# Kernel optimization log

Measured on AMD Instinct MI355X. Metric: run time of the kernel, lower is better.

Reference implementation:

```python
import jax, jax.numpy as jnp
import numpy as np

B, L, D, K = 16, 512, 512, 8
D2 = 2 * D
KS = 9
PAD = (KS - 1) // 2
EPS = 1e-5


def _conv_block(x, w, b, g, beta):
    # x: [B, L, D]; conv over time dim with 'same' padding, then LayerNorm over D, ReLU
    y = jax.lax.conv_general_dilated(
        x.transpose(0, 2, 1), w, window_strides=(1,), padding=[(PAD, PAD)],
        dimension_numbers=('NCH', 'OIH', 'NCH'))
    y = y.transpose(0, 2, 1) + b  # [B, L, D]
    mean = jnp.mean(y, axis=-1, keepdims=True)
    var = jnp.var(y, axis=-1, keepdims=True)
    y = (y - mean) * jax.lax.rsqrt(var + EPS) * g + beta
    return jax.nn.relu(y)


def _gru_scan(x, w_ih, w_hh, b_ih, b_hh):
    # x: [B, L, D]; torch GRUCell math, input = concat(x_t, h_{t-1}) per module
    def step(h, x_t):
        p = jnp.concatenate([x_t, h], axis=-1)          # [B, D + D2]
        gi = p @ w_ih.T + b_ih                          # [B, 3*D2]
        gh = h @ w_hh.T + b_hh
        ir, iz, inn = jnp.split(gi, 3, axis=-1)
        hr, hz, hn = jnp.split(gh, 3, axis=-1)
        r = jax.nn.sigmoid(ir + hr)
        z = jax.nn.sigmoid(iz + hz)
        n = jnp.tanh(inn + r * hn)
        h_new = (1.0 - z) * n + z * h
        return h_new, h_new

    h0 = jnp.zeros((x.shape[0], w_hh.shape[1]), x.dtype)
    _, hs = jax.lax.scan(step, h0, x.transpose(1, 0, 2))  # [L, B, D2]
    return hs.transpose(1, 0, 2)                           # [B, L, D2]


def setup_inputs() -> dict:
    key = jax.random.key(0)
    ks = jax.random.split(key, 12)
    n = lambda k, sh, s=0.02: jax.random.normal(k, sh, dtype=jnp.float32) * s
    return {
        'h_text': jax.random.normal(ks[0], (B, L, D), dtype=jnp.float32),
        'conv1_w': n(ks[1], (D, D, KS)), 'conv1_b': jnp.zeros((D,), jnp.float32),
        'ln1_g': jnp.ones((D,), jnp.float32), 'ln1_b': jnp.zeros((D,), jnp.float32),
        'conv2_w': n(ks[2], (D, D, KS)), 'conv2_b': jnp.zeros((D,), jnp.float32),
        'ln2_g': jnp.ones((D,), jnp.float32), 'ln2_b': jnp.zeros((D,), jnp.float32),
        'w_ih': n(ks[3], (3 * D2, D + D2)), 'w_hh': n(ks[4], (3 * D2, D2)),
        'b_ih': jnp.zeros((3 * D2,), jnp.float32), 'b_hh': jnp.zeros((3 * D2,), jnp.float32),
        'mdn_w_w': n(ks[5], (K, D2)), 'mdn_w_b': jnp.zeros((K,), jnp.float32),
        'mdn_sigma_w': n(ks[6], (K * D2, D2)), 'mdn_sigma_b': jnp.zeros((K * D2,), jnp.float32),
        'mdn_mu_w': n(ks[7], (K * D2, D2)), 'mdn_mu_b': jnp.zeros((K * D2,), jnp.float32),
    }


def reference(h_text, conv1_w, conv1_b, ln1_g, ln1_b, conv2_w, conv2_b, ln2_g, ln2_b,
              w_ih, w_hh, b_ih, b_hh, mdn_w_w, mdn_w_b, mdn_sigma_w, mdn_sigma_b,
              mdn_mu_w, mdn_mu_b):
    x = _conv_block(h_text, conv1_w, conv1_b, ln1_g, ln1_b)
    x = _conv_block(x, conv2_w, conv2_b, ln2_g, ln2_b)
    h = _gru_scan(x, w_ih, w_hh, b_ih, b_hh)                 # [B, L, 2D]
    w = jax.nn.softmax(h @ mdn_w_w.T + mdn_w_b, axis=-1)     # [B, L, K]
    sigma = jnp.exp(h @ mdn_sigma_w.T + mdn_sigma_b).reshape(B, L, K, D2)
    mu = (h @ mdn_mu_w.T + mdn_mu_b).reshape(B, L, K, D2)
    return (w, sigma, mu)
```

## Files before the change

kernel.cpp:

```cpp
#include <hip/hip_runtime.h>
#include <hip/hip_bf16.h>
#include <math.h>

#define BB 16
#define LL 512
#define DD 512
#define DD2 1024
#define KMIX 8
#define LPAD 520
#define GRU_KSTEPS 33

typedef __attribute__((ext_vector_type(8))) short short8;
typedef __attribute__((ext_vector_type(4))) float f32x4;
typedef unsigned short ushort;

__device__ __forceinline__ float bf2f(ushort u) {
  union { float f; unsigned i; } v; v.i = ((unsigned)u) << 16; return v.f;
}
__device__ __forceinline__ ushort f2bf(float f) {
  union { float f; unsigned i; } v; v.f = f;
  unsigned i = v.i;
  unsigned r = i + 0x7FFF + ((i >> 16) & 1);
  return (ushort)(r >> 16);
}

__global__ void k_zero_bf16(ushort* p, long n) {
  for (long i = blockIdx.x * 256 + threadIdx.x; i < n; i += (long)gridDim.x * 256) p[i] = 0;
}
__global__ void k_fill_xpad(const float* __restrict__ x, ushort* __restrict__ xp) {
  const long n = (long)BB * LPAD * DD;
  for (long i = blockIdx.x * 256 + threadIdx.x; i < n; i += (long)gridDim.x * 256) {
    int d = (int)(i & 511);
    long rest = i >> 9;
    int p = (int)(rest % LPAD);
    int b = (int)(rest / LPAD);
    float v = 0.f;
    if (p >= 4 && p < 516) v = x[((long)b * LL + (p - 4)) * DD + d];
    xp[i] = f2bf(v);
  }
}
__global__ void k_pack_convw(const float* __restrict__ w, ushort* __restrict__ wp) {
  const long n = (long)DD * DD * 9;
  for (long idx = blockIdx.x * 256 + threadIdx.x; idx < n; idx += (long)gridDim.x * 256) {
    int i = (int)(idx & 511);
    int o = (int)((idx >> 9) & 511);
    int k = (int)(idx >> 18);
    wp[idx] = f2bf(w[((long)o * DD + i) * 9 + k]);
  }
}
__global__ void k_pack_wihx(const float* __restrict__ w_ih, ushort* __restrict__ wp) {
  const long n = (long)3 * DD2 * DD;
  for (long idx = blockIdx.x * 256 + threadIdx.x; idx < n; idx += (long)gridDim.x * 256) {
    int i = (int)(idx & 511);
    int nr = (int)(idx >> 9);
    wp[idx] = f2bf(w_ih[(long)nr * 1536 + i]);
  }
}
__global__ void k_pack_bf16(const float* __restrict__ s, ushort* __restrict__ d, long n) {
  for (long i = blockIdx.x * 256 + threadIdx.x; i < n; i += (long)gridDim.x * 256) d[i] = f2bf(s[i]);
}
__global__ void k_pack_gru(const float* __restrict__ w_ih, const float* __restrict__ w_hh,
                           const float* __restrict__ b_hh, ushort* __restrict__ wp) {
  const long n = (long)64 * 6 * GRU_KSTEPS * 64 * 8;
  for (long idx = blockIdx.x * 256 + threadIdx.x; idx < n; idx += (long)gridDim.x * 256) {
    int j = (int)(idx & 7);
    int lane = (int)((idx >> 3) & 63);
    long r9 = idx >> 9;
    int ks = (int)(r9 % GRU_KSTEPS);
    long tmp = r9 / GRU_KSTEPS;
    int s = (int)(tmp % 6);
    int blk = (int)(tmp / 6);
    int k = ks * 32 + ((lane >> 4) << 3) + j;
    int u = blk * 16 + (lane & 15);
    float v = 0.f;
    if (s < 3) {
      if (k < 1024) v = w_ih[((long)(s * DD2 + u)) * 1536 + 512 + k];
    } else {
      int nr = (s - 3) * DD2 + u;
      if (k < 1024) v = w_hh[(long)nr * DD2 + k];
      else if (k == 1024) v = b_hh[nr];
    }
    wp[idx] = f2bf(v);
  }
}
__global__ void k_init_hbuf(ushort* hb, unsigned* flags) {
  int i = blockIdx.x * 256 + threadIdx.x;
  if (i < 16384) hb[i] = 0;
  if (i < 1024) flags[i] = 0u;
}

__global__ __launch_bounds__(256) void conv_gemm(
    const ushort* __restrict__ A, const ushort* __restrict__ Bt,
    float* __restrict__ Cout, const float* __restrict__ bias) {
  __shared__ ushort As[64 * 64];
  __shared__ ushort Bs[128 * 64];
  const int tid = threadIdx.x, lane = tid & 63, w = tid >> 6;
  const int wr = w >> 1, wc = w & 1;
  const int m0 = blockIdx.y * 64, n0 = blockIdx.x * 128;
  const int b = m0 >> 9, l = m0 & 511;
  const ushort* Abase = A + ((long)(b * LPAD + l)) * DD;
  const ushort* Bbase = Bt + (long)n0 * DD;

  f32x4 acc[2][4];
#pragma unroll
  for (int m = 0; m < 2; m++)
#pragma unroll
    for (int n = 0; n < 4; n++) acc[m][n] = {0.f, 0.f, 0.f, 0.f};

  for (int seg = 0; seg < 9; ++seg) {
    const ushort* Aseg = Abase + (long)seg * DD;
    const ushort* Bseg = Bbase + (long)seg * DD * DD;
    for (int k0 = 0; k0 < DD; k0 += 64) {
#pragma unroll
      for (int it = 0; it < 2; ++it) {
        int chunk = it * 256 + tid;
        int r = chunk >> 3, cc = chunk & 7, sc = cc ^ (r & 7);
        *(short8*)&As[(size_t)chunk * 8] = *(const short8*)(Aseg + (long)r * DD + k0 + sc * 8);
      }
#pragma unroll
      for (int it = 0; it < 4; ++it) {
        int chunk = it * 256 + tid;
        int r = chunk >> 3, cc = chunk & 7, sc = cc ^ (r & 7);
        *(short8*)&Bs[(size_t)chunk * 8] = *(const short8*)(Bseg + (long)r * DD + k0 + sc * 8);
      }
      __syncthreads();
#pragma unroll
      for (int kk = 0; kk < 2; ++kk) {
        short8 af[2], bfv[4];
#pragma unroll
        for (int m = 0; m < 2; m++) {
          int row = wr * 32 + m * 16 + (lane & 15);
          int ch = (kk * 4 + (lane >> 4)) ^ (row & 7);
          af[m] = *(const short8*)&As[(size_t)(row * 8 + ch) * 8];
        }
#pragma unroll
        for (int nn = 0; nn < 4; nn++) {
          int row = wc * 64 + nn * 16 + (lane & 15);
          int ch = (kk * 4 + (lane >> 4)) ^ (row & 7);
          bfv[nn] = *(const short8*)&Bs[(size_t)(row * 8 + ch) * 8];
        }
#pragma unroll
        for (int m = 0; m < 2; m++)
#pragma unroll
          for (int nn = 0; nn < 4; nn++)
            acc[m][nn] = __builtin_amdgcn_mfma_f32_16x16x32_bf16(af[m], bfv[nn], acc[m][nn], 0, 0, 0);
      }
      __syncthreads();
    }
  }
#pragma unroll
  for (int nn = 0; nn < 4; nn++) {
    const int c = n0 + wc * 64 + nn * 16 + (lane & 15);
    const float bv = bias[c];
#pragma unroll
    for (int m = 0; m < 2; m++) {
      const int rbase = m0 + wr * 32 + m * 16 + ((lane >> 4) << 2);
#pragma unroll
      for (int j = 0; j < 4; j++)
        Cout[(long)(rbase + j) * DD + c] = acc[m][nn][j] + bv;
    }
  }
}

__global__ __launch_bounds__(256) void gix_gemm(
    const ushort* __restrict__ A, const ushort* __restrict__ Bt,
    ushort* __restrict__ Cout, const float* __restrict__ bias) {
  __shared__ ushort As[128 * 64];
  __shared__ ushort Bs[128 * 64];
  const int tid = threadIdx.x, lane = tid & 63, w = tid >> 6;
  const int wr = w >> 1, wc = w & 1;
  const int m0 = blockIdx.y * 128, n0 = blockIdx.x * 128;
  const ushort* Abase = A + (long)m0 * DD;
  const ushort* Bbase = Bt + (long)n0 * DD;

  f32x4 acc[4][4];
#pragma unroll
  for (int i = 0; i < 4; i++)
#pragma unroll
    for (int j = 0; j < 4; j++) acc[i][j] = {0.f, 0.f, 0.f, 0.f};

  for (int k0 = 0; k0 < DD; k0 += 64) {
#pragma unroll
    for (int it = 0; it < 4; ++it) {
      int chunk = it * 256 + tid;
      int r = chunk >> 3, cc = chunk & 7, sc = cc ^ (r & 7);
      *(short8*)&As[(size_t)chunk * 8] = *(const short8*)(Abase + (long)r * DD + k0 + sc * 8);
      *(short8*)&Bs[(size_t)chunk * 8] = *(const short8*)(Bbase + (long)r * DD + k0 + sc * 8);
    }
    __syncthreads();
#pragma unroll
    for (int kk = 0; kk < 2; ++kk) {
      short8 af[4], bfv[4];
#pragma unroll
      for (int m = 0; m < 4; m++) {
        int row = wr * 64 + m * 16 + (lane & 15);
        int ch = (kk * 4 + (lane >> 4)) ^ (row & 7);
        af[m] = *(const short8*)&As[(size_t)(row * 8 + ch) * 8];
      }
#pragma unroll
      for (int nn = 0; nn < 4; nn++) {
        int row = wc * 64 + nn * 16 + (lane & 15);
        int ch = (kk * 4 + (lane >> 4)) ^ (row & 7);
        bfv[nn] = *(const short8*)&Bs[(size_t)(row * 8 + ch) * 8];
      }
#pragma unroll
      for (int m = 0; m < 4; m++)
#pragma unroll
        for (int nn = 0; nn < 4; nn++)
          acc[m][nn] = __builtin_amdgcn_mfma_f32_16x16x32_bf16(af[m], bfv[nn], acc[m][nn], 0, 0, 0);
    }
    __syncthreads();
  }
#pragma unroll
  for (int m = 0; m < 4; m++) {
    int rbase = m0 + wr * 64 + m * 16 + ((lane >> 4) << 2);
#pragma unroll
    for (int nn = 0; nn < 4; nn++) {
      int c = n0 + wc * 64 + nn * 16 + (lane & 15);
      const float bv = bias[c];
#pragma unroll
      for (int j = 0; j < 4; j++) {
        float v = acc[m][nn][j] + bv;
        int r = rbase + j;
        int bb = r >> 9, tt = r & 511, ss = c >> 10, uu = c & 1023;
        long o2 = ((((long)(tt * 64 + (uu >> 4))) * 3 + ss) << 8) + (bb << 4) + (uu & 15);
        Cout[o2] = f2bf(v);
      }
    }
  }
}

template <int DSTPAD>
__global__ __launch_bounds__(256) void ln_relu(
    const float* __restrict__ y, const float* __restrict__ g,
    const float* __restrict__ be, ushort* __restrict__ dst) {
  const int r = blockIdx.x, tid = threadIdx.x;
  float v0 = y[(long)r * DD + tid];
  float v1 = y[(long)r * DD + 256 + tid];
  float s = v0 + v1, sq = v0 * v0 + v1 * v1;
#pragma unroll
  for (int o = 32; o; o >>= 1) { s += __shfl_down(s, o); sq += __shfl_down(sq, o); }
  __shared__ float red[8];
  int w = tid >> 6, lane = tid & 63;
  if (lane == 0) { red[w] = s; red[4 + w] = sq; }
  __syncthreads();
  if (tid == 0) {
    float ts = 0.f, tq = 0.f;
#pragma unroll
    for (int i = 0; i < 4; i++) { ts += red[i]; tq += red[4 + i]; }
    red[0] = ts; red[1] = tq;
  }
  __syncthreads();
  float mean = red[0] * (1.f / 512.f);
  float var = red[1] * (1.f / 512.f) - mean * mean;
  float rs = rsqrtf(var + 1e-5f);
  long dbase;
  if (DSTPAD) { int b = r >> 9, l = r & 511; dbase = ((long)(b * LPAD + l + 4)) * DD; }
  else dbase = (long)r * DD;
  float o0 = fmaxf(0.f, (v0 - mean) * rs * g[tid] + be[tid]);
  float o1 = fmaxf(0.f, (v1 - mean) * rs * g[tid + 256] + be[tid + 256]);
  dst[dbase + tid] = f2bf(o0);
  dst[dbase + 256 + tid] = f2bf(o1);
}

__device__ __forceinline__ void wait_flags(unsigned need, int tid,
                                           const unsigned* __restrict__ flags) {
  if ((tid >> 6) == 0) {
    while (1) {
      unsigned f = __hip_atomic_load(&flags[(tid & 63) << 4], __ATOMIC_RELAXED,
                                     __HIP_MEMORY_SCOPE_AGENT);
      if (__all((int)(f >= need))) break;
      __builtin_amdgcn_s_sleep(127);
    }
  }
  __syncthreads();
}

template <int MR>
__device__ void do_pair(int m0, int n0,
                        const ushort* __restrict__ A,
                        const ushort* __restrict__ Bsg, const ushort* __restrict__ Bmu,
                        const float* __restrict__ sg_b, const float* __restrict__ mu_b,
                        float* __restrict__ Cs, float* __restrict__ Cm,
                        char* smem, int tid) {
  constexpr int NF = (MR == 128) ? 2 : 1;
  ushort* As = (ushort*)smem;
  ushort* B1 = As + MR * 64;
  ushort* B2 = B1 + 128 * 64;
  const int lane = tid & 63, w = tid >> 6;
  const int wr = (MR == 128) ? (w >> 2) : 0;
  const int wc = (MR == 128) ? (w & 3) : w;
  const ushort* Abase = A + (long)m0 * DD2;
  const ushort* Bsb = Bsg + (long)n0 * DD2;
  const ushort* Bmb = Bmu + (long)n0 * DD2;
  f32x4 accS[4][NF], accM[4][NF];
#pragma unroll
  for (int m = 0; m < 4; m++)
#pragma unroll
    for (int n = 0; n < NF; n++) { accS[m][n] = {0.f,0.f,0.f,0.f}; accM[m][n] = {0.f,0.f,0.f,0.f}; }

  for (int k0 = 0; k0 < DD2; k0 += 64) {
#pragma unroll
    for (int it = 0; it < MR / 64; ++it) {
      int chunk = it * 512 + tid;
      int r = chunk >> 3, cc = chunk & 7, sc = cc ^ (r & 7);
      *(short8*)&As[(size_t)chunk * 8] = *(const short8*)(Abase + (long)r * DD2 + k0 + sc * 8);
    }
#pragma unroll
    for (int it = 0; it < 2; ++it) {
      int chunk = it * 512 + tid;
      int r = chunk >> 3, cc = chunk & 7, sc = cc ^ (r & 7);
      *(short8*)&B1[(size_t)chunk * 8] = *(const short8*)(Bsb + (long)r * DD2 + k0 + sc * 8);
      *(short8*)&B2[(size_t)chunk * 8] = *(const short8*)(Bmb + (long)r * DD2 + k0 + sc * 8);
    }
    __syncthreads();
#pragma unroll
    for (int kk = 0; kk < 2; ++kk) {
      short8 af[4], b1[NF], b2[NF];
#pragma unroll
      for (int m = 0; m < 4; m++) {
        int row = wr * 64 + m * 16 + (lane & 15);
        int ch = (kk * 4 + (lane >> 4)) ^ (row & 7);
        af[m] = *(const short8*)&As[(size_t)(row * 8 + ch) * 8];
      }
#pragma unroll
      for (int n = 0; n < NF; n++) {
        int row = wc * (16 * NF) + n * 16 + (lane & 15);
        int ch = (kk * 4 + (lane >> 4)) ^ (row & 7);
        b1[n] = *(const short8*)&B1[(size_t)(row * 8 + ch) * 8];
        b2[n] = *(const short8*)&B2[(size_t)(row * 8 + ch) * 8];
      }
#pragma unroll
      for (int m = 0; m < 4; m++)
#pragma unroll
        for (int n = 0; n < NF; n++) {
          accS[m][n] = __builtin_amdgcn_mfma_f32_16x16x32_bf16(af[m], b1[n], accS[m][n], 0, 0, 0);
          accM[m][n] = __builtin_amdgcn_mfma_f32_16x16x32_bf16(af[m], b2[n], accM[m][n], 0, 0, 0);
        }
    }
    __syncthreads();
  }
  const int ldc = KMIX * DD2;
#pragma unroll
  for (int n = 0; n < NF; n++) {
    const int c = n0 + wc * (16 * NF) + n * 16 + (lane & 15);
    const float bs = sg_b[c], bm = mu_b[c];
#pragma unroll
    for (int m = 0; m < 4; m++) {
      const int rbase = m0 + wr * 64 + m * 16 + ((lane >> 4) << 2);
#pragma unroll
      for (int j = 0; j < 4; j++) {
        const long off = (long)(rbase + j) * ldc + c;
        Cs[off] = expf(accS[m][n][j] + bs);
        Cm[off] = accM[m][n][j] + bm;
      }
    }
  }
}

__global__ __launch_bounds__(512, 2) void fused_scan_mdn(
    const ushort* __restrict__ Wp, const ushort* __restrict__ gix2,
    const float* __restrict__ b_hh,
    ushort* __restrict__ hbuf, ushort* __restrict__ h_seq,
    unsigned* __restrict__ flags,
    const ushort* __restrict__ mdnsg, const ushort* __restrict__ mdnmu,
    const float* __restrict__ sg_b, const float* __restrict__ mu_b,
    float* __restrict__ outS, float* __restrict__ outM,
    const float* __restrict__ ww, const float* __restrict__ wb,
    float* __restrict__ outW) {
  __shared__ char smem[49152];
  const int tid = threadIdx.x;

  if (blockIdx.x < 64) {
    float* red = (float*)smem;
    const int lane = tid & 63, w = tid >> 6, blk = blockIdx.x;
    const int j_c = w;
    const int u_local = lane & 15;
    const int b = ((lane >> 4) << 2) + (j_c & 3);
    const int u = (blk << 4) + u_local;
    const int lanep = ((blk & 1) * 2 + (u_local >> 3)) * 16 + b;
    const long hout_off = ((long)(blk >> 1) * 64 + lanep) * 8 + (u_local & 7);
    const ushort* wpw = Wp + (long)blk * 6 * GRU_KSTEPS * 512 + (long)lane * 8;
    const float bhr = b_hh[u], bhz = b_hh[DD2 + u], bhn = b_hh[2 * DD2 + u];
    float hold = 0.f;

    short8 wr0[4], wr1[4], wr2[4], wr3[4], wr4[4], wr5[4];
#pragma unroll
    for (int i = 0; i < 4; ++i) {
      const int ks = i * 8 + w;
      wr0[i] = *(const short8*)(wpw + (long)(0 * GRU_KSTEPS + ks) * 512);
      wr1[i] = *(const short8*)(wpw + (long)(1 * GRU_KSTEPS + ks) * 512);
      wr2[i] = *(const short8*)(wpw + (long)(2 * GRU_KSTEPS + ks) * 512);
      wr3[i] = *(const short8*)(wpw + (long)(3 * GRU_KSTEPS + ks) * 512);
      wr4[i] = *(const short8*)(wpw + (long)(4 * GRU_KSTEPS + ks) * 512);
      wr5[i] = *(const short8*)(wpw + (long)(5 * GRU_KSTEPS + ks) * 512);
    }

    const int gofs = (b << 4) + u_local;
    for (int t = 0; t < LL; ++t) {
      float gx_r = 0.f, gx_z = 0.f, gx_n = 0.f;
      if (w < 4) {
        const long gbase = ((long)(t * 64 + blk) * 3) << 8;
        gx_r = bf2f(__builtin_nontemporal_load(gix2 + gbase + gofs));
        gx_z = bf2f(__builtin_nontemporal_load(gix2 + gbase + 256 + gofs));
        gx_n = bf2f(__builtin_nontemporal_load(gix2 + gbase + 512 + gofs));
      }
      if (t > 0) {
        if (w == 0) {
          const unsigned tgt = (unsigned)t;
          while (1) {
            unsigned f = __hip_atomic_load(&flags[lane << 4], __ATOMIC_RELAXED,
                                           __HIP_MEMORY_SCOPE_AGENT);
            if (__all((int)(f >= tgt))) break;
            __builtin_amdgcn_s_sleep(1);
          }
        }
        __syncthreads();
      }

      const ushort* hb = hbuf + ((long)t << 14);
      f32x4 acc0 = {0.f,0.f,0.f,0.f}, acc1 = acc0, acc2 = acc0,
            acc3 = acc0, acc4 = acc0, acc5 = acc0;
#pragma unroll
      for (int i = 0; i < 4; ++i) {
        const int ks = i * 8 + w;
        unsigned long long* ap = (unsigned long long*)(hb + (((long)ks * 64 + lane) << 3));
        union { unsigned long long q[2]; short8 v; } cv;
        cv.q[0] = __hip_atomic_load(ap,     __ATOMIC_RELAXED, __HIP_MEMORY_SCOPE_AGENT);
        cv.q[1] = __hip_atomic_load(ap + 1, __ATOMIC_RELAXED, __HIP_MEMORY_SCOPE_AGENT);
        acc0 = __builtin_amdgcn_mfma_f32_16x16x32_bf16(cv.v, wr0[i], acc0, 0, 0, 0);
        acc1 = __builtin_amdgcn_mfma_f32_16x16x32_bf16(cv.v, wr1[i], acc1, 0, 0, 0);
        acc2 = __builtin_amdgcn_mfma_f32_16x16x32_bf16(cv.v, wr2[i], acc2, 0, 0, 0);
        acc3 = __builtin_amdgcn_mfma_f32_16x16x32_bf16(cv.v, wr3[i], acc3, 0, 0, 0);
        acc4 = __builtin_amdgcn_mfma_f32_16x16x32_bf16(cv.v, wr4[i], acc4, 0, 0, 0);
        acc5 = __builtin_amdgcn_mfma_f32_16x16x32_bf16(cv.v, wr5[i], acc5, 0, 0, 0);
      }
#pragma unroll
      for (int j = 0; j < 4; ++j) {
        red[((w * 6 + 0) << 8) + (j << 6) + lane] = acc0[j];
        red[((w * 6 + 1) << 8) + (j << 6) + lane] = acc1[j];
        red[((w * 6 + 2) << 8) + (j << 6) + lane] = acc2[j];
        red[((w * 6 + 3) << 8) + (j << 6) + lane] = acc3[j];
        red[((w * 6 + 4) << 8) + (j << 6) + lane] = acc4[j];
        red[((w * 6 + 5) << 8) + (j << 6) + lane] = acc5[j];
      }
      __syncthreads();
      ushort h16 = 0;
      if (w < 4) {
        float v0 = 0.f, v1 = 0.f, v2 = 0.f, v3 = 0.f, v4 = 0.f, v5 = 0.f;
#pragma unroll
        for (int wv = 0; wv < 8; ++wv) {
          const int base = ((wv * 6) << 8) + (j_c << 6) + lane;
          v0 += red[base];
          v1 += red[base + 256];
          v2 += red[base + 512];
          v3 += red[base + 768];
          v4 += red[base + 1024];
          v5 += red[base + 1280];
        }
        const float rg = 1.f / (1.f + __expf(-(gx_r + v0 + v3 + bhr)));
        const float zg = 1.f / (1.f + __expf(-(gx_z + v1 + v4 + bhz)));
        const float nx = gx_n + v2 + rg * (v5 + bhn);
        const float ng = 1.f - 2.f / (__expf(2.f * nx) + 1.f);
        const float hn = (1.f - zg) * ng + zg * hold;
        hold = hn;
        h16 = f2bf(hn);
      }
      if (t < LL - 1) {
        if (w < 4)
          __hip_atomic_store(hbuf + (((long)(t + 1)) << 14) + hout_off, h16,
                             __ATOMIC_RELAXED, __HIP_MEMORY_SCOPE_AGENT);
        __syncthreads();
        if (tid == 0)
          __hip_atomic_store(&flags[blk << 4], (unsigned)(t + 1), __ATOMIC_RELAXED,
                             __HIP_MEMORY_SCOPE_AGENT);
      }
      if (w < 4)
        __hip_atomic_store(h_seq + ((long)b * LL + t) * DD2 + u, h16,
                           __ATOMIC_RELAXED, __HIP_MEMORY_SCOPE_AGENT);
    }
    __syncthreads();
    if (tid == 0)
      __hip_atomic_store(&flags[blk << 4], 600u, __ATOMIC_RELAXED,
                         __HIP_MEMORY_SCOPE_AGENT);
  } else {
    const int wid = blockIdx.x - 64;
    for (int i = wid; i < 3072; i += 192) {
      const int nb = i & 63;
      const int rest = i >> 6;
      const int b = rest & 15;
      const int t0 = (rest >> 4) * 128;
      wait_flags((unsigned)(t0 + 129), tid, flags);
      do_pair<128>(b * 512 + t0, nb * 128, h_seq, mdnsg, mdnmu, sg_b, mu_b,
                   outS, outM, smem, tid);
    }
    for (int i = wid; i < 1024; i += 192) {
      const int nb = i & 63;
      const int b = (i >> 6) & 15;
      wait_flags(449u, tid, flags);
      do_pair<64>(b * 512 + 384, nb * 128, h_seq, mdnsg, mdnmu, sg_b, mu_b,
                  outS, outM, smem, tid);
    }
  }
  for (int i = blockIdx.x; i < 1024; i += 256) {
    const int nb = i & 63;
    const int b = (i >> 6) & 15;
    wait_flags(513u, tid, flags);
    do_pair<64>(b * 512 + 448, nb * 128, h_seq, mdnsg, mdnmu, sg_b, mu_b,
                outS, outM, smem, tid);
  }
  wait_flags(513u, tid, flags);
  {
    const int lane = tid & 63, w = tid >> 6;
#pragma unroll
    for (int i = 0; i < 4; ++i) {
      const long r = (long)blockIdx.x * 32 + i * 8 + w;
      float s[KMIX];
#pragma unroll
      for (int k = 0; k < KMIX; k++) s[k] = 0.f;
      for (int u = lane; u < DD2; u += 64) {
        float hv = bf2f(h_seq[r * DD2 + u]);
#pragma unroll
        for (int k = 0; k < KMIX; k++) s[k] += hv * ww[(long)k * DD2 + u];
      }
#pragma unroll
      for (int k = 0; k < KMIX; k++)
#pragma unroll
        for (int o = 32; o; o >>= 1) s[k] += __shfl_xor(s[k], o);
#pragma unroll
      for (int k = 0; k < KMIX; k++) s[k] += wb[k];
      float m = s[0];
#pragma unroll
      for (int k = 1; k < KMIX; k++) m = fmaxf(m, s[k]);
      float esum = 0.f;
#pragma unroll
      for (int k = 0; k < KMIX; k++) { s[k] = expf(s[k] - m); esum += s[k]; }
      float mine = 0.f;
#pragma unroll
      for (int k = 0; k < KMIX; k++) if (lane == k) mine = s[k];
      if (lane < KMIX) outW[r * KMIX + lane] = mine / esum;
    }
  }
}

extern "C" void kernel_launch(void* const* d_in, const int* in_sizes, int n_in,
                              void* d_out, int out_size, void* d_ws, size_t ws_size,
                              hipStream_t stream) {
  const float* h_text     = (const float*)d_in[0];
  const float* conv1_w    = (const float*)d_in[1];
  const float* conv1_b    = (const float*)d_in[2];
  const float* ln1_g      = (const float*)d_in[3];
  const float* ln1_b      = (const float*)d_in[4];
  const float* conv2_w    = (const float*)d_in[5];
  const float* conv2_b    = (const float*)d_in[6];
  const float* ln2_g      = (const float*)d_in[7];
  const float* ln2_b      = (const float*)d_in[8];
  const float* w_ih       = (const float*)d_in[9];
  const float* w_hh       = (const float*)d_in[10];
  const float* b_ih       = (const float*)d_in[11];
  const float* b_hh       = (const float*)d_in[12];
  const float* mdn_w_w    = (const float*)d_in[13];
  const float* mdn_w_b    = (const float*)d_in[14];
  const float* mdn_sig_w  = (const float*)d_in[15];
  const float* mdn_sig_b  = (const float*)d_in[16];
  const float* mdn_mu_w   = (const float*)d_in[17];
  const float* mdn_mu_b   = (const float*)d_in[18];
  float* out = (float*)d_out;

  char* ws = (char*)d_ws;
  size_t off = 0;
  auto take = [&](size_t bytes) {
    void* p = ws + off;
    off += (bytes + 255) & ~(size_t)255;
    return p;
  };
  ushort* xpad1  = (ushort*)take((size_t)BB * LPAD * DD * 2);
  ushort* xpad2  = (ushort*)take((size_t)BB * LPAD * DD * 2);
  ushort* wpack1 = (ushort*)take((size_t)DD * DD * 9 * 2);
  ushort* wpack2 = (ushort*)take((size_t)DD * DD * 9 * 2);
  float*  ybuf   = (float*) take((size_t)BB * LL * DD * 4);
  ushort* x2     = (ushort*)take((size_t)BB * LL * DD * 2);
  ushort* wihx   = (ushort*)take((size_t)3 * DD2 * DD * 2);
  ushort* gix    = (ushort*)take((size_t)BB * LL * 3 * DD2 * 2);
  ushort* Wp     = (ushort*)take((size_t)64 * 6 * GRU_KSTEPS * 64 * 8 * 2);
  ushort* hseq   = (ushort*)take((size_t)BB * LL * DD2 * 2);
  ushort* mdnmu  = (ushort*)take((size_t)KMIX * DD2 * DD2 * 2);
  ushort* mdnsg  = (ushort*)take((size_t)KMIX * DD2 * DD2 * 2);
  ushort* hbuf   = (ushort*)take((size_t)512 * 16384 * 2);
  unsigned* flags = (unsigned*)take(64 * 16 * 4);

  const long sigma_off = (long)BB * LL * KMIX;
  const long mu_off    = sigma_off + (long)BB * LL * KMIX * DD2;

  k_fill_xpad<<<2048, 256, 0, stream>>>(h_text, xpad1);
  k_zero_bf16<<<2048, 256, 0, stream>>>(xpad2, (long)BB * LPAD * DD);
  k_pack_convw<<<2048, 256, 0, stream>>>(conv1_w, wpack1);
  k_pack_convw<<<2048, 256, 0, stream>>>(conv2_w, wpack2);
  k_pack_wihx<<<2048, 256, 0, stream>>>(w_ih, wihx);
  k_pack_gru<<<2048, 256, 0, stream>>>(w_ih, w_hh, b_hh, Wp);
  k_pack_bf16<<<2048, 256, 0, stream>>>(mdn_mu_w, mdnmu, (long)KMIX * DD2 * DD2);
  k_pack_bf16<<<2048, 256, 0, stream>>>(mdn_sig_w, mdnsg, (long)KMIX * DD2 * DD2);
  k_init_hbuf<<<64, 256, 0, stream>>>(hbuf, flags);

  conv_gemm<<<dim3(4, 128), 256, 0, stream>>>(xpad1, wpack1, ybuf, conv1_b);
  ln_relu<1><<<BB * LL, 256, 0, stream>>>(ybuf, ln1_g, ln1_b, xpad2);

  conv_gemm<<<dim3(4, 128), 256, 0, stream>>>(xpad2, wpack2, ybuf, conv2_b);
  ln_relu<0><<<BB * LL, 256, 0, stream>>>(ybuf, ln2_g, ln2_b, x2);

  gix_gemm<<<dim3(24, 64), 256, 0, stream>>>(x2, wihx, gix, b_ih);

  fused_scan_mdn<<<256, 512, 0, stream>>>(Wp, gix, b_hh, hbuf, hseq, flags,
                                          mdnsg, mdnmu, mdn_sig_b, mdn_mu_b,
                                          out + sigma_off, out + mu_off,
                                          mdn_w_w, mdn_w_b, out);
}
```

Baseline: 1.682 ms.

## Use per-wave progress flags in GRU recurrence to drop block barrier

Each of the four producing waves now publishes its own progress flag after its h store drains (s_waitcnt vmcnt(0)), instead of the whole block meeting at a __syncthreads and thread 0 writing a single flag. Consumers read the four per-wave flags in each 64-byte line with two 64-bit atomic loads and require all of them to be ready. This removes one block barrier from the serial per-timestep critical path of the recurrence. The final wait_flags before the mixture-weight softmax stage is also dropped, which relies on the earlier do_pair waits already guaranteeing completion; any ordering mistake here would be a correctness risk.

```diff
diff --git a/kernel.cpp b/kernel.cpp
--- a/kernel.cpp
+++ b/kernel.cpp
@@ -263,13 +263,24 @@
   dst[dbase + 256 + tid] = f2bf(o1);
 }
 
+__device__ __forceinline__ bool line_ok(const unsigned* __restrict__ flags,
+                                        int blkline, unsigned need) {
+  unsigned long long q0 = __hip_atomic_load(
+      (const unsigned long long*)&flags[blkline << 4],
+      __ATOMIC_RELAXED, __HIP_MEMORY_SCOPE_AGENT);
+  unsigned long long q1 = __hip_atomic_load(
+      (const unsigned long long*)&flags[(blkline << 4) + 2],
+      __ATOMIC_RELAXED, __HIP_MEMORY_SCOPE_AGENT);
+  const unsigned m0 = (unsigned)q0, m1 = (unsigned)(q0 >> 32);
+  const unsigned m2 = (unsigned)q1, m3 = (unsigned)(q1 >> 32);
+  return (m0 >= need) & (m1 >= need) & (m2 >= need) & (m3 >= need);
+}
+
 __device__ __forceinline__ void wait_flags(unsigned need, int tid,
                                            const unsigned* __restrict__ flags) {
   if ((tid >> 6) == 0) {
     while (1) {
-      unsigned f = __hip_atomic_load(&flags[(tid & 63) << 4], __ATOMIC_RELAXED,
-                                     __HIP_MEMORY_SCOPE_AGENT);
-      if (__all((int)(f >= need))) break;
+      if (__all((int)line_ok(flags, tid & 63, need))) break;
       __builtin_amdgcn_s_sleep(127);
     }
   }
@@ -409,9 +420,7 @@
         if (w == 0) {
           const unsigned tgt = (unsigned)t;
           while (1) {
-            unsigned f = __hip_atomic_load(&flags[lane << 4], __ATOMIC_RELAXED,
-                                           __HIP_MEMORY_SCOPE_AGENT);
-            if (__all((int)(f >= tgt))) break;
+            if (__all((int)line_ok(flags, lane, tgt))) break;
             __builtin_amdgcn_s_sleep(1);
           }
         }
@@ -445,7 +454,6 @@
         red[((w * 6 + 5) << 8) + (j << 6) + lane] = acc5[j];
       }
       __syncthreads();
-      ushort h16 = 0;
       if (w < 4) {
         float v0 = 0.f, v1 = 0.f, v2 = 0.f, v3 = 0.f, v4 = 0.f, v5 = 0.f;
 #pragma unroll
@@ -464,25 +472,25 @@
         const float ng = 1.f - 2.f / (__expf(2.f * nx) + 1.f);
         const float hn = (1.f - zg) * ng + zg * hold;
         hold = hn;
-        h16 = f2bf(hn);
-      }
-      if (t < LL - 1) {
-        if (w < 4)
+        const ushort h16 = f2bf(hn);
+        if (t < LL - 1) {
           __hip_atomic_store(hbuf + (((long)(t + 1)) << 14) + hout_off, h16,
                              __ATOMIC_RELAXED, __HIP_MEMORY_SCOPE_AGENT);
-        __syncthreads();
-        if (tid == 0)
-          __hip_atomic_store(&flags[blk << 4], (unsigned)(t + 1), __ATOMIC_RELAXED,
-                             __HIP_MEMORY_SCOPE_AGENT);
-      }
-      if (w < 4)
+          asm volatile("s_waitcnt vmcnt(0)" ::: "memory");
+          if (lane == 0)
+            __hip_atomic_store(&flags[(blk << 4) + w], (unsigned)(t + 1),
+                               __ATOMIC_RELAXED, __HIP_MEMORY_SCOPE_AGENT);
+        }
         __hip_atomic_store(h_seq + ((long)b * LL + t) * DD2 + u, h16,
                            __ATOMIC_RELAXED, __HIP_MEMORY_SCOPE_AGENT);
-    }
-    __syncthreads();
-    if (tid == 0)
-      __hip_atomic_store(&flags[blk << 4], 600u, __ATOMIC_RELAXED,
-                         __HIP_MEMORY_SCOPE_AGENT);
+      }
+    }
+    if (w < 4) {
+      asm volatile("s_waitcnt vmcnt(0)" ::: "memory");
+      if (lane == 0)
+        __hip_atomic_store(&flags[(blk << 4) + w], 600u, __ATOMIC_RELAXED,
+                           __HIP_MEMORY_SCOPE_AGENT);
+    }
   } else {
     const int wid = blockIdx.x - 64;
     for (int i = wid; i < 3072; i += 192) {
@@ -509,7 +517,6 @@
     do_pair<64>(b * 512 + 448, nb * 128, h_seq, mdnsg, mdnmu, sg_b, mu_b,
                 outS, outM, smem, tid);
   }
-  wait_flags(513u, tid, flags);
   {
     const int lane = tid & 63, w = tid >> 6;
 #pragma unroll
```

After: 2.161 ms. 1.28x slower.
